# Kernel optimization log

Measured on AMD Instinct MI355X. Metric: run time of the kernel, lower is better.

Reference implementation:

```python
import jax, jax.numpy as jnp
from jax import lax
import numpy as np

RNN = 512; FC = 512; COND = 128; FEAT = 80; NCLS = 256; HALF = RNN // 2
PAD = 2; SCALES = (5, 5, 11); MEL_T = 86  # -> 22550 output samples


def setup_inputs() -> dict:
    key = jax.random.key(0)
    ks = jax.random.split(key, 12)
    s = 0.05
    p = {"mels": jax.random.normal(ks[0], (1, FEAT, MEL_T), jnp.float32)}
    ch = FEAT
    for i, sc in enumerate(SCALES):
        k = 2 * sc + 1
        p[f"up_w{i}"] = jax.random.normal(ks[1 + i], (COND, ch, k), jnp.float32) * s
        p[f"up_b{i}"] = jnp.zeros((COND,), jnp.float32)
        ch = COND
    p["Wx"] = jax.random.normal(ks[4], (3 * RNN, 3 + COND), jnp.float32) * s
    p["bx"] = jnp.zeros((3 * RNN,), jnp.float32)
    p["Wh"] = jax.random.normal(ks[5], (3 * RNN, RNN), jnp.float32) * s
    p["bh"] = jnp.zeros((3 * RNN,), jnp.float32)
    p["O1w"] = jax.random.normal(ks[6], (FC, HALF), jnp.float32) * s
    p["O1b"] = jnp.zeros((FC,), jnp.float32)
    p["O2w"] = jax.random.normal(ks[7], (NCLS, FC), jnp.float32) * s
    p["O2b"] = jnp.zeros((NCLS,), jnp.float32)
    p["O3w"] = jax.random.normal(ks[8], (FC, HALF), jnp.float32) * s
    p["O3b"] = jnp.zeros((FC,), jnp.float32)
    p["O4w"] = jax.random.normal(ks[9], (NCLS, FC), jnp.float32) * s
    p["O4b"] = jnp.zeros((NCLS,), jnp.float32)
    return p


def _upsample(mels, ws, bs):
    # mels[:, :, excess_pad:-excess_pad] with excess_pad = PAD - 1 = 1
    x = mels[:, :, PAD - 1:-(PAD - 1)]
    for w, b, sc in zip(ws, bs, SCALES):
        k = 2 * sc + 1
        # ConvTranspose1d(stride=sc, kernel=k, padding=(3*sc-1)//2) as an
        # input-dilated conv: edge pad = k-1-torch_pad = (sc+1)//2
        e = k - 1 - (3 * sc - 1) // 2
        x = lax.conv_general_dilated(x, w, window_strides=(1,),
                                     padding=[(e, e)], lhs_dilation=(sc,),
                                     dimension_numbers=('NCH', 'OIH', 'NCH'))
        x = jax.nn.relu(x + b[None, :, None])
    return x[0, :, 1:-1].T  # [T, COND]


def _gru(inp, h, Wx, bx, Wh, bh):
    xg = Wx @ inp + bx
    hg = Wh @ h + bh
    xr, xz, xn = jnp.split(xg, 3)
    hr, hz, hn = jnp.split(hg, 3)
    r = jax.nn.sigmoid(xr + hr)
    z = jax.nn.sigmoid(xz + hz)
    n = jnp.tanh(xn + r * hn)
    return (1.0 - z) * n + z * h


def reference(mels, up_w0, up_b0, up_w1, up_b1, up_w2, up_b2,
              Wx, bx, Wh, bh, O1w, O1b, O2w, O2b, O3w, O3b, O4w, O4b):
    cond = _upsample(mels, (up_w0, up_w1, up_w2), (up_b0, up_b1, up_b2))
    zero = jnp.float32(0.0)

    def step(carry, m_t):
        h, c_val, f_val = carry
        # coarse pass: x = [c_{t-1}, f_{t-1}, 0]
        inp1 = jnp.concatenate([jnp.stack([c_val, f_val, zero]), m_t])
        h1 = _gru(inp1, h, Wx, bx, Wh, bh)
        oc = O2w @ jax.nn.relu(O1w @ h1[:HALF] + O1b) + O2b
        c_cat = jnp.argmax(oc).astype(jnp.float32)  # deterministic=True path
        c_new = c_cat / 127.5 - 1.0
        # fine pass: x = [c_{t-1}, f_{t-1}, c_t]
        inp2 = jnp.concatenate([jnp.stack([c_val, f_val, c_new]), m_t])
        h2 = _gru(inp2, h, Wx, bx, Wh, bh)
        of = O4w @ jax.nn.relu(O3w @ h2[HALF:] + O3b) + O4b
        f_cat = jnp.argmax(of).astype(jnp.float32)
        f_new = f_cat / 127.5 - 1.0
        sample = (c_cat * 256.0 + f_cat) / 32767.5 - 1.0
        return (h2, c_new, f_new), (sample, jnp.concatenate([oc, of]))

    init = (jnp.zeros((RNN,), jnp.float32), zero, zero)
    _, (samples, logits) = lax.scan(step, init, cond)
    return samples, logits  # [T], [T, 512]
```

## Files before the change

kernel.cpp:

```cpp
#include <hip/hip_runtime.h>
#include <math.h>

#define T_STEPS 22550
#define NWG 32
#define NTHR 256

typedef unsigned long long ull;

#define SL_PRE  0
#define SL_O1   2048
#define SL_O3   2560
#define SL_AM1  3072
#define SL_AM2  3104
#define SL_END  3168

#define OF_SLOT  64
#define OF_AFTER (OF_SLOT + SL_END*2)
#define OF_BUFA  OF_AFTER
#define OF_BUFB  (OF_BUFA + 128*412)
#define OF_COND  (OF_BUFB + 128*2052)

__global__ void k_init(float* ws){
  int i = blockIdx.x*blockDim.x + threadIdx.x;
  ull* sl = (ull*)(ws + OF_SLOT);
  if (i < SL_END) __hip_atomic_store(&sl[i], 0ULL, __ATOMIC_RELAXED, __HIP_MEMORY_SCOPE_AGENT);
}

__global__ void k_upconv(const float* __restrict__ x, int instride, int inoff,
                         const float* __restrict__ w, const float* __restrict__ b,
                         float* __restrict__ y, int Cin, int Lin, int K, int sc, int e,
                         int Lout, int mode)
{
  int j = blockIdx.x*blockDim.x + threadIdx.x;
  int c = blockIdx.y;
  if (j >= Lout) return;
  float acc = b[c];
  int kstart = ((e - j) % sc + sc) % sc;
  for (int i = 0; i < Cin; ++i){
    const float* wci = w + (c*Cin + i)*K;
    const float* xi  = x + i*instride + inoff;
    for (int k = kstart; k < K; k += sc){
      int qd = j - e + k;
      if (qd >= 0){
        int qq = qd / sc;
        if (qq < Lin) acc += wci[k]*xi[qq];
      }
    }
  }
  acc = fmaxf(acc, 0.f);
  if (mode == 0) y[c*Lout + j] = acc;
  else { int t = j - 1; if (t >= 0 && t < T_STEPS) y[t*128 + c] = acc; }
}

__device__ __forceinline__ float sigm(float x){ return 1.f/(1.f + expf(-x)); }

__device__ __forceinline__ void pub64(ull* p, ull pk){
  (void)__hip_atomic_exchange(p, pk, __ATOMIC_RELAXED, __HIP_MEMORY_SCOPE_AGENT);
}
__device__ __forceinline__ ull ld64(ull* p){
  return __hip_atomic_load(p, __ATOMIC_RELAXED, __HIP_MEMORY_SCOPE_AGENT);
}
__device__ __forceinline__ float spin_data(ull* p, unsigned tag){
  ull pk = ld64(p);
  while ((unsigned)pk != tag) pk = ld64(p);
  return __uint_as_float((unsigned)(pk >> 32));
}
__device__ __forceinline__ ull spin_am(ull* p, unsigned tag){
  ull pk = ld64(p);
  while ((unsigned)(pk & 0xFFFFFFu) != tag) pk = ld64(p);
  return pk;
}
__device__ __forceinline__ ull pack_data(float v, unsigned tag){
  return ((ull)__float_as_uint(v) << 32) | (ull)tag;
}

__launch_bounds__(NTHR)
__global__ void k_wavernn(const float* __restrict__ Wx, const float* __restrict__ bx,
                          const float* __restrict__ Wh, const float* __restrict__ bh,
                          const float* __restrict__ O1w, const float* __restrict__ O1b,
                          const float* __restrict__ O2w, const float* __restrict__ O2b,
                          const float* __restrict__ O3w, const float* __restrict__ O3b,
                          const float* __restrict__ O4w, const float* __restrict__ O4b,
                          float* ws, float* __restrict__ out)
{
  __shared__ __align__(16) float h_s[512];
  __shared__ __align__(16) float m_s[128];
  __shared__ __align__(16) float h1_s[256];
  __shared__ __align__(16) float o_s[512];
  __shared__ __align__(16) float pr_s[512], pz_s[512], pna_s[512], hn_s[512];
  __shared__ __align__(16) float w1r_s[512], w1z_s[512], w1n_s[512];
  __shared__ __align__(16) float w2r_s[512], w2z_s[512], w2n_s[512];
  __shared__ float hg_s[48], xgb_s[48];
  __shared__ float red_s[8], sc_s[8];
  __shared__ float wc0_s[48], bx_s[48], bh_s[48];

  const int tid = threadIdx.x, g = blockIdx.x;
  ull* sl = (ull*)(ws + OF_SLOT);
  const float* cond = ws + OF_COND;
  float* out_samp = out;
  float* out_log  = out + T_STEPS;

  if (tid < 48){
    int row = (tid>>4)*512 + g + 32*(tid&15);
    wc0_s[tid] = Wx[(size_t)row*131 + 0];
    bx_s[tid]  = bx[row];
    bh_s[tid]  = bh[row];
  }
  for (int e = tid; e < 512; e += NTHR){
    w1r_s[e] = Wx[(size_t)e*131 + 1];
    w1z_s[e] = Wx[(size_t)(512+e)*131 + 1];
    w1n_s[e] = Wx[(size_t)(1024+e)*131 + 1];
    w2r_s[e] = Wx[(size_t)e*131 + 2];
    w2z_s[e] = Wx[(size_t)(512+e)*131 + 2];
    w2n_s[e] = Wx[(size_t)(1024+e)*131 + 2];
  }
  const int m16 = tid>>4, c16 = tid&15;
  const int rowO1 = g + 32*m16;
  float wO1r[16], wO3r[16];
  #pragma unroll
  for (int k=0;k<16;++k){
    wO1r[k] = O1w[(size_t)rowO1*256 + c16*16 + k];
    wO3r[k] = O3w[(size_t)rowO1*256 + c16*16 + k];
  }
  const float bO1r = O1b[rowO1], bO3r = O3b[rowO1];
  const int m8 = tid>>5, l32 = tid&31;
  const int row2 = g + 32*m8;
  float wO2r[16], wO4r[16];
  #pragma unroll
  for (int k=0;k<16;++k){
    wO2r[k] = O2w[(size_t)row2*512 + l32 + 32*k];
    wO4r[k] = O4w[(size_t)row2*512 + l32 + 32*k];
  }
  const float bO2 = O2b[row2], bO4 = O4b[row2];

  h_s[tid] = 0.f; h_s[tid+256] = 0.f;
  if (tid < 128) m_s[tid] = cond[tid];
  if (tid == 0){ sc_s[0] = 0.f; sc_s[2] = 0.f; sc_s[3] = 0.f; }
  __syncthreads();

  #define COMPUTE_WX() do { \
    if (tid < 192){ \
      const int li_ = tid>>2, q_ = tid&3; \
      const int row_ = (li_>>4)*512 + g + 32*(li_&15); \
      const float* WxR = Wx + (size_t)row_*131 + 3; \
      float aX = 0.f; \
      _Pragma("unroll") \
      for (int kk=0; kk<32; ++kk){ \
        int f_ = q_*32 + ((kk + 8*q_) & 31); \
        aX += WxR[f_]*m_s[f_]; \
      } \
      aX += __shfl_xor(aX,1); aX += __shfl_xor(aX,2); \
      if (q_ == 0) xgb_s[li_] = aX + bx_s[li_]; \
    } } while(0)

  #define COMPUTE_WH() do { \
    if (tid < 192){ \
      const int li_ = tid>>2, q_ = tid&3; \
      const int row_ = (li_>>4)*512 + g + 32*(li_&15); \
      const float4* W4 = (const float4*)(Wh + (size_t)row_*512); \
      const float4* H4 = (const float4*)h_s; \
      float aH = 0.f; \
      _Pragma("unroll") \
      for (int kk=0; kk<32; ++kk){ \
        int f_ = q_*32 + ((kk + 2*q_) & 31); \
        float4 w = W4[f_], v = H4[f_]; \
        aH += w.x*v.x + w.y*v.y + w.z*v.z + w.w*v.w; \
      } \
      aH += __shfl_xor(aH,1); aH += __shfl_xor(aH,2); \
      if (q_ == 0) hg_s[li_] = aH + bh_s[li_]; \
    } } while(0)

  #define PUB_PREGATES(TAGP) do { \
    if (tid < 64){ \
      const int i_ = tid>>2, c_ = tid&3; \
      const int e_ = g + 32*i_; \
      const float c0_ = sc_s[3]; \
      float v_; \
      if (c_ == 0)      v_ = xgb_s[i_]    + c0_*wc0_s[i_]    + hg_s[i_]; \
      else if (c_ == 1) v_ = xgb_s[16+i_] + c0_*wc0_s[16+i_] + hg_s[16+i_]; \
      else if (c_ == 2) v_ = xgb_s[32+i_] + c0_*wc0_s[32+i_]; \
      else              v_ = hg_s[32+i_]; \
      pub64(&sl[SL_PRE + e_*4 + c_], pack_data(v_, (TAGP))); \
    } } while(0)

  COMPUTE_WX();
  if (tid < 48) hg_s[tid] = bh_s[tid];
  __syncthreads();
  PUB_PREGATES(1u);

  for (int t = 0; t < T_STEPS; ++t){
    const unsigned tag = (unsigned)(t + 1);

    {
      ull pk[8];
      #pragma unroll
      for (int c=0;c<4;++c){
        pk[c]   = ld64(&sl[SL_PRE + tid*4 + c]);
        pk[4+c] = ld64(&sl[SL_PRE + (tid+256)*4 + c]);
      }
      bool all;
      do {
        all = true;
        #pragma unroll
        for (int i=0;i<8;++i){
          if ((unsigned)pk[i] != tag){
            int slot = (i<4) ? (tid*4 + i) : ((tid+256)*4 + (i-4));
            pk[i] = ld64(&sl[SL_PRE + slot]);
            if ((unsigned)pk[i] != tag) all = false;
          }
        }
      } while (!all);
      pr_s[tid]      = __uint_as_float((unsigned)(pk[0] >> 32));
      pz_s[tid]      = __uint_as_float((unsigned)(pk[1] >> 32));
      pna_s[tid]     = __uint_as_float((unsigned)(pk[2] >> 32));
      hn_s[tid]      = __uint_as_float((unsigned)(pk[3] >> 32));
      pr_s[tid+256]  = __uint_as_float((unsigned)(pk[4] >> 32));
      pz_s[tid+256]  = __uint_as_float((unsigned)(pk[5] >> 32));
      pna_s[tid+256] = __uint_as_float((unsigned)(pk[6] >> 32));
      hn_s[tid+256]  = __uint_as_float((unsigned)(pk[7] >> 32));
    }
    if (t > 0 && tid < 32){
      ull pk = spin_am(&sl[SL_AM2 + ((t-1) & 1)*32 + tid], tag - 1);
      float bv = __uint_as_float((unsigned)(pk >> 32));
      int   bi = (int)((pk >> 24) & 0xFFu);
      #pragma unroll
      for (int off=16; off>=1; off>>=1){
        float ov = __shfl_xor(bv,off); int oi = __shfl_xor(bi,off);
        if (ov > bv || (ov == bv && oi < bi)){ bv = ov; bi = oi; }
      }
      if (tid == 0){
        sc_s[0] = (float)bi/127.5f - 1.f;
        if (g == 0) out_samp[t-1] = (sc_s[2]*256.f + (float)bi)/32767.5f - 1.f;
      }
    }
    if (tid < 128 && t + 1 < T_STEPS) m_s[tid] = cond[(size_t)(t+1)*128 + tid];
    __syncthreads();

    {
      const float f = sc_s[0];
      float r = sigm(pr_s[tid]  + f*w1r_s[tid]);
      float z = sigm(pz_s[tid]  + f*w1z_s[tid]);
      float n = tanhf(pna_s[tid] + f*w1n_s[tid] + r*hn_s[tid]);
      h1_s[tid] = (1.f - z)*n + z*h_s[tid];
    }
    __syncthreads();

    {
      float acc = 0.f;
      #pragma unroll
      for (int k=0;k<16;++k) acc += wO1r[k]*h1_s[c16*16 + k];
      acc += __shfl_xor(acc,1); acc += __shfl_xor(acc,2);
      acc += __shfl_xor(acc,4); acc += __shfl_xor(acc,8);
      if (c16 == 0) pub64(&sl[SL_O1 + g*16 + m16], pack_data(fmaxf(acc + bO1r, 0.f), tag));
    }
    COMPUTE_WX();
    o_s[tid]       = spin_data(&sl[SL_O1 + (tid & 31)*16 + (tid >> 5)], tag);
    o_s[tid + 256] = spin_data(&sl[SL_O1 + (tid & 31)*16 + (tid >> 5) + 8], tag);
    __syncthreads();

    {
      float acc = 0.f;
      #pragma unroll
      for (int k=0;k<16;++k) acc += wO2r[k]*o_s[l32 + 32*k];
      acc += __shfl_xor(acc,1); acc += __shfl_xor(acc,2); acc += __shfl_xor(acc,4);
      acc += __shfl_xor(acc,8); acc += __shfl_xor(acc,16);
      if (l32 == 0){ float v = acc + bO2; out_log[(size_t)t*512 + row2] = v; red_s[m8] = v; }
    }
    __syncthreads();
    if (tid == 0){
      float bv = red_s[0]; int bi = g;
      #pragma unroll
      for (int m=1;m<8;++m){ float v = red_s[m]; if (v > bv){ bv = v; bi = g + 32*m; } }
      pub64(&sl[SL_AM1 + g],
            ((ull)__float_as_uint(bv) << 32) | ((ull)(unsigned)bi << 24) | tag);
    }
    if (tid < 32){
      ull pk = spin_am(&sl[SL_AM1 + tid], tag);
      float bv = __uint_as_float((unsigned)(pk >> 32));
      int   bi = (int)((pk >> 24) & 0xFFu);
      #pragma unroll
      for (int off=16; off>=1; off>>=1){
        float ov = __shfl_xor(bv,off); int oi = __shfl_xor(bi,off);
        if (ov > bv || (ov == bv && oi < bi)){ bv = ov; bi = oi; }
      }
      if (tid == 0){ sc_s[2] = (float)bi; sc_s[3] = (float)bi/127.5f - 1.f; }
    }
    __syncthreads();

    {
      const float f = sc_s[0], cn = sc_s[3];
      #pragma unroll
      for (int hh=0; hh<2; ++hh){
        int e = tid + 256*hh;
        float r = sigm(pr_s[e]  + f*w1r_s[e] + cn*w2r_s[e]);
        float z = sigm(pz_s[e]  + f*w1z_s[e] + cn*w2z_s[e]);
        float n = tanhf(pna_s[e] + f*w1n_s[e] + cn*w2n_s[e] + r*hn_s[e]);
        h_s[e] = (1.f - z)*n + z*h_s[e];
      }
    }
    __syncthreads();

    {
      float acc = 0.f;
      #pragma unroll
      for (int k=0;k<16;++k) acc += wO3r[k]*h_s[256 + c16*16 + k];
      acc += __shfl_xor(acc,1); acc += __shfl_xor(acc,2);
      acc += __shfl_xor(acc,4); acc += __shfl_xor(acc,8);
      if (c16 == 0) pub64(&sl[SL_O3 + g*16 + m16], pack_data(fmaxf(acc + bO3r, 0.f), tag));
    }
    COMPUTE_WH();
    __syncthreads();
    if (t + 1 < T_STEPS) PUB_PREGATES((unsigned)(t + 2));
    o_s[tid]       = spin_data(&sl[SL_O3 + (tid & 31)*16 + (tid >> 5)], tag);
    o_s[tid + 256] = spin_data(&sl[SL_O3 + (tid & 31)*16 + (tid >> 5) + 8], tag);
    __syncthreads();

    {
      float acc = 0.f;
      #pragma unroll
      for (int k=0;k<16;++k) acc += wO4r[k]*o_s[l32 + 32*k];
      acc += __shfl_xor(acc,1); acc += __shfl_xor(acc,2); acc += __shfl_xor(acc,4);
      acc += __shfl_xor(acc,8); acc += __shfl_xor(acc,16);
      if (l32 == 0){ float v = acc + bO4; out_log[(size_t)t*512 + 256 + row2] = v; red_s[m8] = v; }
    }
    __syncthreads();
    if (tid == 0){
      float bv = red_s[0]; int bi = g;
      #pragma unroll
      for (int m=1;m<8;++m){ float v = red_s[m]; if (v > bv){ bv = v; bi = g + 32*m; } }
      pub64(&sl[SL_AM2 + (t & 1)*32 + g],
            ((ull)__float_as_uint(bv) << 32) | ((ull)(unsigned)bi << 24) | tag);
    }
  }

  if (g == 0 && tid < 32){
    ull pk = spin_am(&sl[SL_AM2 + ((T_STEPS-1) & 1)*32 + tid], (unsigned)T_STEPS);
    float bv = __uint_as_float((unsigned)(pk >> 32));
    int   bi = (int)((pk >> 24) & 0xFFu);
    #pragma unroll
    for (int off=16; off>=1; off>>=1){
      float ov = __shfl_xor(bv,off); int oi = __shfl_xor(bi,off);
      if (ov > bv || (ov == bv && oi < bi)){ bv = ov; bi = oi; }
    }
    if (tid == 0) out_samp[T_STEPS-1] = (sc_s[2]*256.f + (float)bi)/32767.5f - 1.f;
  }
}

extern "C" void kernel_launch(void* const* d_in, const int* in_sizes, int n_in,
                              void* d_out, int out_size, void* d_ws, size_t ws_size,
                              hipStream_t stream)
{
  const float* mels  = (const float*)d_in[0];
  const float* up_w0 = (const float*)d_in[1]; const float* up_b0 = (const float*)d_in[2];
  const float* up_w1 = (const float*)d_in[3]; const float* up_b1 = (const float*)d_in[4];
  const float* up_w2 = (const float*)d_in[5]; const float* up_b2 = (const float*)d_in[6];
  const float* Wx  = (const float*)d_in[7];  const float* bx  = (const float*)d_in[8];
  const float* Wh  = (const float*)d_in[9];  const float* bh  = (const float*)d_in[10];
  const float* O1w = (const float*)d_in[11]; const float* O1b = (const float*)d_in[12];
  const float* O2w = (const float*)d_in[13]; const float* O2b = (const float*)d_in[14];
  const float* O3w = (const float*)d_in[15]; const float* O3b = (const float*)d_in[16];
  const float* O4w = (const float*)d_in[17]; const float* O4b = (const float*)d_in[18];
  float* ws  = (float*)d_ws;
  float* out = (float*)d_out;

  k_init<<<(SL_END + 255)/256, 256, 0, stream>>>(ws);

  k_upconv<<<dim3((412  +127)/128, 128), 128, 0, stream>>>(mels,        86,   1, up_w0, up_b0,
            ws+OF_BUFA,  80,   84, 11,  5, 3,   412, 0);
  k_upconv<<<dim3((2052 +127)/128, 128), 128, 0, stream>>>(ws+OF_BUFA, 412,   0, up_w1, up_b1,
            ws+OF_BUFB, 128,  412, 11,  5, 3,  2052, 0);
  k_upconv<<<dim3((22552+127)/128, 128), 128, 0, stream>>>(ws+OF_BUFB, 2052,  0, up_w2, up_b2,
            ws+OF_COND, 128, 2052, 23, 11, 6, 22552, 1);

  k_wavernn<<<NWG, NTHR, 0, stream>>>(Wx, bx, Wh, bh, O1w, O1b, O2w, O2b,
                                      O3w, O3b, O4w, O4b, ws, out);
}
```

Before: 295.9 ms.

## Replace two-phase O2/O4 exchange with partial-logit all-gather and local argmax

Each workgroup now multiplies its own 16 O1/O3 hidden units by the matching O2/O4 weight columns and publishes 256 partial logits. Every workgroup then gathers all 32 partials per logit and computes the full logits and argmax locally. This replaces the former chain of publishing hidden activations, spinning, computing logit slices, publishing per-group argmax and spinning again, cutting one cross-workgroup synchronisation round per pass. In exchange, each thread polls 32 slots per pass, which adds memory traffic and register pressure, and every group redundantly reduces all 256 logits.

```diff
diff --git a/kernel.cpp b/kernel.cpp
--- a/kernel.cpp
+++ b/kernel.cpp
@@ -8,11 +8,9 @@
 typedef unsigned long long ull;
 
 #define SL_PRE  0
-#define SL_O1   2048
-#define SL_O3   2560
-#define SL_AM1  3072
-#define SL_AM2  3104
-#define SL_END  3168
+#define SL_PLC  2048
+#define SL_PLF  10240
+#define SL_END  18432
 
 #define OF_SLOT  64
 #define OF_AFTER (OF_SLOT + SL_END*2)
@@ -60,16 +58,6 @@
 __device__ __forceinline__ ull ld64(ull* p){
   return __hip_atomic_load(p, __ATOMIC_RELAXED, __HIP_MEMORY_SCOPE_AGENT);
 }
-__device__ __forceinline__ float spin_data(ull* p, unsigned tag){
-  ull pk = ld64(p);
-  while ((unsigned)pk != tag) pk = ld64(p);
-  return __uint_as_float((unsigned)(pk >> 32));
-}
-__device__ __forceinline__ ull spin_am(ull* p, unsigned tag){
-  ull pk = ld64(p);
-  while ((unsigned)(pk & 0xFFFFFFu) != tag) pk = ld64(p);
-  return pk;
-}
 __device__ __forceinline__ ull pack_data(float v, unsigned tag){
   return ((ull)__float_as_uint(v) << 32) | (ull)tag;
 }
@@ -86,12 +74,13 @@
   __shared__ __align__(16) float h_s[512];
   __shared__ __align__(16) float m_s[128];
   __shared__ __align__(16) float h1_s[256];
-  __shared__ __align__(16) float o_s[512];
+  __shared__ __align__(16) float logit_s[256];
   __shared__ __align__(16) float pr_s[512], pz_s[512], pna_s[512], hn_s[512];
   __shared__ __align__(16) float w1r_s[512], w1z_s[512], w1n_s[512];
   __shared__ __align__(16) float w2r_s[512], w2z_s[512], w2n_s[512];
+  __shared__ float o1own_s[16], o3own_s[16];
   __shared__ float hg_s[48], xgb_s[48];
-  __shared__ float red_s[8], sc_s[8];
+  __shared__ float sc_s[8];
   __shared__ float wc0_s[48], bx_s[48], bh_s[48];
 
   const int tid = threadIdx.x, g = blockIdx.x;
@@ -123,15 +112,13 @@
     wO3r[k] = O3w[(size_t)rowO1*256 + c16*16 + k];
   }
   const float bO1r = O1b[rowO1], bO3r = O3b[rowO1];
-  const int m8 = tid>>5, l32 = tid&31;
-  const int row2 = g + 32*m8;
-  float wO2r[16], wO4r[16];
+  float wPC[16], wPF[16];
   #pragma unroll
-  for (int k=0;k<16;++k){
-    wO2r[k] = O2w[(size_t)row2*512 + l32 + 32*k];
-    wO4r[k] = O4w[(size_t)row2*512 + l32 + 32*k];
-  }
-  const float bO2 = O2b[row2], bO4 = O4b[row2];
+  for (int m=0;m<16;++m){
+    wPC[m] = O2w[(size_t)tid*512 + g + 32*m];
+    wPF[m] = O4w[(size_t)tid*512 + g + 32*m];
+  }
+  const float cbO2 = O2b[tid], cbO4 = O4b[tid];
 
   h_s[tid] = 0.f; h_s[tid+256] = 0.f;
   if (tid < 128) m_s[tid] = cond[tid];
@@ -183,6 +170,25 @@
       pub64(&sl[SL_PRE + e_*4 + c_], pack_data(v_, (TAGP))); \
     } } while(0)
 
+  #define FAT_GATHER(BASE, BIAS) do { \
+    ull pk_[32]; \
+    _Pragma("unroll") \
+    for (int g2=0; g2<32; ++g2) pk_[g2] = ld64(&sl[(BASE) + g2*256 + tid]); \
+    for (;;){ \
+      bool all_ = true; \
+      _Pragma("unroll") \
+      for (int g2=0; g2<32; ++g2) if ((unsigned)pk_[g2] != tag) all_ = false; \
+      if (all_) break; \
+      _Pragma("unroll") \
+      for (int g2=0; g2<32; ++g2) \
+        if ((unsigned)pk_[g2] != tag) pk_[g2] = ld64(&sl[(BASE) + g2*256 + tid]); \
+    } \
+    float s_ = (BIAS); \
+    _Pragma("unroll") \
+    for (int g2=0; g2<32; ++g2) s_ += __uint_as_float((unsigned)(pk_[g2] >> 32)); \
+    logit_s[tid] = s_; \
+  } while(0)
+
   COMPUTE_WX();
   if (tid < 48) hg_s[tid] = bh_s[tid];
   __syncthreads();
@@ -198,18 +204,18 @@
         pk[c]   = ld64(&sl[SL_PRE + tid*4 + c]);
         pk[4+c] = ld64(&sl[SL_PRE + (tid+256)*4 + c]);
       }
-      bool all;
-      do {
-        all = true;
+      for (;;){
+        bool all = true;
         #pragma unroll
-        for (int i=0;i<8;++i){
+        for (int i=0;i<8;++i) if ((unsigned)pk[i] != tag) all = false;
+        if (all) break;
+        #pragma unroll
+        for (int i=0;i<8;++i)
           if ((unsigned)pk[i] != tag){
             int slot = (i<4) ? (tid*4 + i) : ((tid+256)*4 + (i-4));
             pk[i] = ld64(&sl[SL_PRE + slot]);
-            if ((unsigned)pk[i] != tag) all = false;
           }
-        }
-      } while (!all);
+      }
       pr_s[tid]      = __uint_as_float((unsigned)(pk[0] >> 32));
       pz_s[tid]      = __uint_as_float((unsigned)(pk[1] >> 32));
       pna_s[tid]     = __uint_as_float((unsigned)(pk[2] >> 32));
@@ -219,20 +225,6 @@
       pna_s[tid+256] = __uint_as_float((unsigned)(pk[6] >> 32));
       hn_s[tid+256]  = __uint_as_float((unsigned)(pk[7] >> 32));
     }
-    if (t > 0 && tid < 32){
-      ull pk = spin_am(&sl[SL_AM2 + ((t-1) & 1)*32 + tid], tag - 1);
-      float bv = __uint_as_float((unsigned)(pk >> 32));
-      int   bi = (int)((pk >> 24) & 0xFFu);
-      #pragma unroll
-      for (int off=16; off>=1; off>>=1){
-        float ov = __shfl_xor(bv,off); int oi = __shfl_xor(bi,off);
-        if (ov > bv || (ov == bv && oi < bi)){ bv = ov; bi = oi; }
-      }
-      if (tid == 0){
-        sc_s[0] = (float)bi/127.5f - 1.f;
-        if (g == 0) out_samp[t-1] = (sc_s[2]*256.f + (float)bi)/32767.5f - 1.f;
-      }
-    }
     if (tid < 128 && t + 1 < T_STEPS) m_s[tid] = cond[(size_t)(t+1)*128 + tid];
     __syncthreads();
 
@@ -251,35 +243,27 @@
       for (int k=0;k<16;++k) acc += wO1r[k]*h1_s[c16*16 + k];
       acc += __shfl_xor(acc,1); acc += __shfl_xor(acc,2);
       acc += __shfl_xor(acc,4); acc += __shfl_xor(acc,8);
-      if (c16 == 0) pub64(&sl[SL_O1 + g*16 + m16], pack_data(fmaxf(acc + bO1r, 0.f), tag));
-    }
+      if (c16 == 0) o1own_s[m16] = fmaxf(acc + bO1r, 0.f);
+    }
+    __syncthreads();
+    {
+      float s = 0.f;
+      #pragma unroll
+      for (int m=0;m<16;++m) s += wPC[m]*o1own_s[m];
+      pub64(&sl[SL_PLC + g*256 + tid], pack_data(s, tag));
+    }
+
     COMPUTE_WX();
-    o_s[tid]       = spin_data(&sl[SL_O1 + (tid & 31)*16 + (tid >> 5)], tag);
-    o_s[tid + 256] = spin_data(&sl[SL_O1 + (tid & 31)*16 + (tid >> 5) + 8], tag);
-    __syncthreads();
-
-    {
-      float acc = 0.f;
-      #pragma unroll
-      for (int k=0;k<16;++k) acc += wO2r[k]*o_s[l32 + 32*k];
-      acc += __shfl_xor(acc,1); acc += __shfl_xor(acc,2); acc += __shfl_xor(acc,4);
-      acc += __shfl_xor(acc,8); acc += __shfl_xor(acc,16);
-      if (l32 == 0){ float v = acc + bO2; out_log[(size_t)t*512 + row2] = v; red_s[m8] = v; }
-    }
-    __syncthreads();
-    if (tid == 0){
-      float bv = red_s[0]; int bi = g;
-      #pragma unroll
-      for (int m=1;m<8;++m){ float v = red_s[m]; if (v > bv){ bv = v; bi = g + 32*m; } }
-      pub64(&sl[SL_AM1 + g],
-            ((ull)__float_as_uint(bv) << 32) | ((ull)(unsigned)bi << 24) | tag);
-    }
-    if (tid < 32){
-      ull pk = spin_am(&sl[SL_AM1 + tid], tag);
-      float bv = __uint_as_float((unsigned)(pk >> 32));
-      int   bi = (int)((pk >> 24) & 0xFFu);
-      #pragma unroll
-      for (int off=16; off>=1; off>>=1){
+
+    FAT_GATHER(SL_PLC, cbO2);
+    __syncthreads();
+    if (tid < 8) out_log[(size_t)t*512 + g*8 + tid] = logit_s[g*8 + tid];
+    if (tid < 64){
+      float bv = logit_s[tid]; int bi = tid;
+      #pragma unroll
+      for (int j=1;j<4;++j){ float v = logit_s[tid + 64*j]; if (v > bv){ bv = v; bi = tid + 64*j; } }
+      #pragma unroll
+      for (int off=32; off>=1; off>>=1){
         float ov = __shfl_xor(bv,off); int oi = __shfl_xor(bi,off);
         if (ov > bv || (ov == bv && oi < bi)){ bv = ov; bi = oi; }
       }
@@ -306,43 +290,37 @@
       for (int k=0;k<16;++k) acc += wO3r[k]*h_s[256 + c16*16 + k];
       acc += __shfl_xor(acc,1); acc += __shfl_xor(acc,2);
       acc += __shfl_xor(acc,4); acc += __shfl_xor(acc,8);
-      if (c16 == 0) pub64(&sl[SL_O3 + g*16 + m16], pack_data(fmaxf(acc + bO3r, 0.f), tag));
-    }
+      if (c16 == 0) o3own_s[m16] = fmaxf(acc + bO3r, 0.f);
+    }
+    __syncthreads();
+    {
+      float s = 0.f;
+      #pragma unroll
+      for (int m=0;m<16;++m) s += wPF[m]*o3own_s[m];
+      pub64(&sl[SL_PLF + g*256 + tid], pack_data(s, tag));
+    }
+
     COMPUTE_WH();
     __syncthreads();
     if (t + 1 < T_STEPS) PUB_PREGATES((unsigned)(t + 2));
-    o_s[tid]       = spin_data(&sl[SL_O3 + (tid & 31)*16 + (tid >> 5)], tag);
-    o_s[tid + 256] = spin_data(&sl[SL_O3 + (tid & 31)*16 + (tid >> 5) + 8], tag);
-    __syncthreads();
-
-    {
-      float acc = 0.f;
-      #pragma unroll
-      for (int k=0;k<16;++k) acc += wO4r[k]*o_s[l32 + 32*k];
-      acc += __shfl_xor(acc,1); acc += __shfl_xor(acc,2); acc += __shfl_xor(acc,4);
-      acc += __shfl_xor(acc,8); acc += __shfl_xor(acc,16);
-      if (l32 == 0){ float v = acc + bO4; out_log[(size_t)t*512 + 256 + row2] = v; red_s[m8] = v; }
-    }
-    __syncthreads();
-    if (tid == 0){
-      float bv = red_s[0]; int bi = g;
-      #pragma unroll
-      for (int m=1;m<8;++m){ float v = red_s[m]; if (v > bv){ bv = v; bi = g + 32*m; } }
-      pub64(&sl[SL_AM2 + (t & 1)*32 + g],
-            ((ull)__float_as_uint(bv) << 32) | ((ull)(unsigned)bi << 24) | tag);
-    }
-  }
-
-  if (g == 0 && tid < 32){
-    ull pk = spin_am(&sl[SL_AM2 + ((T_STEPS-1) & 1)*32 + tid], (unsigned)T_STEPS);
-    float bv = __uint_as_float((unsigned)(pk >> 32));
-    int   bi = (int)((pk >> 24) & 0xFFu);
-    #pragma unroll
-    for (int off=16; off>=1; off>>=1){
-      float ov = __shfl_xor(bv,off); int oi = __shfl_xor(bi,off);
-      if (ov > bv || (ov == bv && oi < bi)){ bv = ov; bi = oi; }
-    }
-    if (tid == 0) out_samp[T_STEPS-1] = (sc_s[2]*256.f + (float)bi)/32767.5f - 1.f;
+
+    FAT_GATHER(SL_PLF, cbO4);
+    __syncthreads();
+    if (tid < 8) out_log[(size_t)t*512 + 256 + g*8 + tid] = logit_s[g*8 + tid];
+    if (tid < 64){
+      float bv = logit_s[tid]; int bi = tid;
+      #pragma unroll
+      for (int j=1;j<4;++j){ float v = logit_s[tid + 64*j]; if (v > bv){ bv = v; bi = tid + 64*j; } }
+      #pragma unroll
+      for (int off=32; off>=1; off>>=1){
+        float ov = __shfl_xor(bv,off); int oi = __shfl_xor(bi,off);
+        if (ov > bv || (ov == bv && oi < bi)){ bv = ov; bi = oi; }
+      }
+      if (tid == 0){
+        sc_s[0] = (float)bi/127.5f - 1.f;
+        if (g == 0) out_samp[t] = (sc_s[2]*256.f + (float)bi)/32767.5f - 1.f;
+      }
+    }
   }
 }
 
```

Measured after the change: 295.9 ms. About the same (+0.0%).

## Co-locate persistent team on one XCD and spin on L2 with sc0 loads

Applied to the files above, without the earlier changes.

The launch now uses 256 workgroups, reads each block's XCC id from a hardware register, and elects the 32 blocks that share one XCC as the working team; the other blocks exit. When the team shares an XCC, the flag exchanges use non-coherent sc0 global loads and stores, meant to be served by that XCC's shared L2 instead of device-coherent memory. Every publish is also mirrored to an agent-scope atomic slot, which readers poll occasionally as a fallback. A generation counter replaces zeroing the flag slots on each launch. This targets the cross-workgroup handoff latency of the serial recurrence, at the cost of a startup election and handshake and a dependence on sc0 behaviour and on how blocks are placed across XCCs.

```diff
diff --git a/kernel.cpp b/kernel.cpp
--- a/kernel.cpp
+++ b/kernel.cpp
@@ -4,26 +4,39 @@
 #define T_STEPS 22550
 #define NWG 32
 #define NTHR 256
+#define GRID 256
 
 typedef unsigned long long ull;
+typedef unsigned int uint4v __attribute__((ext_vector_type(4)));
 
 #define SL_PRE  0
 #define SL_O1   2048
 #define SL_O3   2560
 #define SL_AM1  3072
 #define SL_AM2  3104
-#define SL_END  3168
-
-#define OF_SLOT  64
-#define OF_AFTER (OF_SLOT + SL_END*2)
-#define OF_BUFA  OF_AFTER
+#define SL_VER  3168
+#define SL_TOT  3200
+
+#define OF_GEN   8
+#define OF_ELEC  16
+#define OF_ARR   64
+#define OF_VOTE  320
+#define OF_FAST  384
+#define OF_MIR   6784
+#define OF_BUFA  13184
 #define OF_BUFB  (OF_BUFA + 128*412)
 #define OF_COND  (OF_BUFB + 128*2052)
 
 __global__ void k_init(float* ws){
   int i = blockIdx.x*blockDim.x + threadIdx.x;
-  ull* sl = (ull*)(ws + OF_SLOT);
-  if (i < SL_END) __hip_atomic_store(&sl[i], 0ULL, __ATOMIC_RELAXED, __HIP_MEMORY_SCOPE_AGENT);
+  if (i == 0){
+    unsigned* gen = (unsigned*)(ws + OF_GEN);
+    unsigned g = (__hip_atomic_load(gen, __ATOMIC_RELAXED, __HIP_MEMORY_SCOPE_AGENT) + 1u) & 0xFFFFFFu;
+    if (g == 0) g = 1;
+    __hip_atomic_store(gen, g, __ATOMIC_RELAXED, __HIP_MEMORY_SCOPE_AGENT);
+  }
+  if (i >= 8 && i < 16)
+    __hip_atomic_store((int*)(ws + OF_ELEC) + (i - 8), 0, __ATOMIC_RELAXED, __HIP_MEMORY_SCOPE_AGENT);
 }
 
 __global__ void k_upconv(const float* __restrict__ x, int instride, int inoff,
@@ -54,24 +67,78 @@
 
 __device__ __forceinline__ float sigm(float x){ return 1.f/(1.f + expf(-x)); }
 
-__device__ __forceinline__ void pub64(ull* p, ull pk){
-  (void)__hip_atomic_exchange(p, pk, __ATOMIC_RELAXED, __HIP_MEMORY_SCOPE_AGENT);
-}
-__device__ __forceinline__ ull ld64(ull* p){
-  return __hip_atomic_load(p, __ATOMIC_RELAXED, __HIP_MEMORY_SCOPE_AGENT);
-}
-__device__ __forceinline__ float spin_data(ull* p, unsigned tag){
-  ull pk = ld64(p);
-  while ((unsigned)pk != tag) pk = ld64(p);
-  return __uint_as_float((unsigned)(pk >> 32));
-}
-__device__ __forceinline__ ull spin_am(ull* p, unsigned tag){
-  ull pk = ld64(p);
-  while ((unsigned)(pk & 0xFFFFFFu) != tag) pk = ld64(p);
-  return pk;
+__device__ __forceinline__ ull ld64_f(const ull* p){
+  ull r;
+  asm volatile("global_load_dwordx2 %0, %1, off sc0\n\ts_waitcnt vmcnt(0)"
+               : "=&v"(r) : "v"(p) : "memory");
+  return r;
+}
+__device__ __forceinline__ void ld2_f(const ull* p0, const ull* p1, ull& a, ull& b){
+  asm volatile("global_load_dwordx2 %0, %2, off sc0\n\t"
+               "global_load_dwordx2 %1, %3, off sc0\n\t"
+               "s_waitcnt vmcnt(0)"
+               : "=&v"(a), "=&v"(b) : "v"(p0), "v"(p1) : "memory");
+}
+__device__ __forceinline__ void ld4_f(const ull* p, ull pk[4]){
+  uint4v a, b;
+  asm volatile("global_load_dwordx4 %0, %2, off sc0\n\t"
+               "global_load_dwordx4 %1, %3, off sc0\n\t"
+               "s_waitcnt vmcnt(0)"
+               : "=&v"(a), "=&v"(b) : "v"(p), "v"(p + 2) : "memory");
+  pk[0] = ((ull)a.y << 32) | a.x;  pk[1] = ((ull)a.w << 32) | a.z;
+  pk[2] = ((ull)b.y << 32) | b.x;  pk[3] = ((ull)b.w << 32) | b.z;
+}
+__device__ __forceinline__ void st64_f(ull* p, ull v){
+  asm volatile("global_store_dwordx2 %0, %1, off sc0" :: "v"(p), "v"(v) : "memory");
+}
+__device__ __forceinline__ ull ld64_a(const ull* p){
+  return __hip_atomic_load((ull*)p, __ATOMIC_RELAXED, __HIP_MEMORY_SCOPE_AGENT);
+}
+__device__ __forceinline__ void pub_dual(ull* f, ull* m, ull pk){
+  st64_f(f, pk);
+  __hip_atomic_store(m, pk, __ATOMIC_RELAXED, __HIP_MEMORY_SCOPE_AGENT);
 }
 __device__ __forceinline__ ull pack_data(float v, unsigned tag){
   return ((ull)__float_as_uint(v) << 32) | (ull)tag;
+}
+__device__ __forceinline__ ull spin_am_dual(ull* f, ull* m, unsigned tag, bool FM){
+  if (FM){
+    int it = 0;
+    for (;;){
+      ull pk = ld64_f(f);
+      if ((unsigned)(pk & 0xFFFFFFu) == tag) return pk;
+      if (((++it) & 15) == 0){
+        pk = ld64_a(m);
+        if ((unsigned)(pk & 0xFFFFFFu) == tag) return pk;
+      }
+    }
+  }
+  ull pk = ld64_a(m);
+  while ((unsigned)(pk & 0xFFFFFFu) != tag) pk = ld64_a(m);
+  return pk;
+}
+__device__ __forceinline__ void spin2_dual(ull* f0, ull* f1, ull* m0, ull* m1,
+                                           unsigned tag, bool FM, float& r0, float& r1){
+  ull v0 = 0, v1 = 0; unsigned done = 0;
+  if (FM){
+    int it = 0;
+    while (done != 3u){
+      ull a, b; ld2_f(f0, f1, a, b);
+      if (!(done & 1) && (unsigned)a == tag){ v0 = a; done |= 1; }
+      if (!(done & 2) && (unsigned)b == tag){ v1 = b; done |= 2; }
+      if (((++it) & 15) == 0){
+        if (!(done & 1)){ ull q = ld64_a(m0); if ((unsigned)q == tag){ v0 = q; done |= 1; } }
+        if (!(done & 2)){ ull q = ld64_a(m1); if ((unsigned)q == tag){ v1 = q; done |= 2; } }
+      }
+    }
+  } else {
+    while (done != 3u){
+      if (!(done & 1)){ ull q = ld64_a(m0); if ((unsigned)q == tag){ v0 = q; done |= 1; } }
+      if (!(done & 2)){ ull q = ld64_a(m1); if ((unsigned)q == tag){ v1 = q; done |= 2; } }
+    }
+  }
+  r0 = __uint_as_float((unsigned)(v0 >> 32));
+  r1 = __uint_as_float((unsigned)(v1 >> 32));
 }
 
 __launch_bounds__(NTHR)
@@ -93,12 +160,77 @@
   __shared__ float hg_s[48], xgb_s[48];
   __shared__ float red_s[8], sc_s[8];
   __shared__ float wc0_s[48], bx_s[48], bh_s[48];
-
-  const int tid = threadIdx.x, g = blockIdx.x;
-  ull* sl = (ull*)(ws + OF_SLOT);
+  __shared__ unsigned gen_sh;
+  __shared__ int team_sh, fastc_sh, saw_sh, fm_sh, myxcc_sh, myslot_sh;
+  __shared__ int cnt_sh[8];
+
+  const int tid = threadIdx.x;
+  int* elec = (int*)(ws + OF_ELEC);
+  unsigned* arr = (unsigned*)(ws + OF_ARR);
+  unsigned* vote = (unsigned*)(ws + OF_VOTE);
+  ull* fA = (ull*)(ws + OF_FAST);
+  ull* mA = (ull*)(ws + OF_MIR);
   const float* cond = ws + OF_COND;
   float* out_samp = out;
   float* out_log  = out + T_STEPS;
+
+  if (tid == 0){
+    gen_sh = __hip_atomic_load((unsigned*)(ws + OF_GEN), __ATOMIC_RELAXED, __HIP_MEMORY_SCOPE_AGENT);
+    unsigned xcc;
+    asm volatile("s_getreg_b32 %0, hwreg(20, 0, 4)" : "=s"(xcc));
+    myxcc_sh = (int)(xcc & 7u);
+    myslot_sh = __hip_atomic_fetch_add(&elec[xcc & 7u], 1, __ATOMIC_RELAXED, __HIP_MEMORY_SCOPE_AGENT);
+    __hip_atomic_store(&arr[blockIdx.x], gen_sh, __ATOMIC_RELAXED, __HIP_MEMORY_SCOPE_AGENT);
+  }
+  __syncthreads();
+  {
+    unsigned v;
+    do { v = __hip_atomic_load(&arr[tid], __ATOMIC_RELAXED, __HIP_MEMORY_SCOPE_AGENT); }
+    while (v != gen_sh);
+  }
+  __syncthreads();
+  if (tid < 8) cnt_sh[tid] = __hip_atomic_load(&elec[tid], __ATOMIC_RELAXED, __HIP_MEMORY_SCOPE_AGENT);
+  __syncthreads();
+  if (tid == 0){
+    int w = 0, c = -1;
+    for (int x = 0; x < 8; ++x) if (cnt_sh[x] > c){ c = cnt_sh[x]; w = x; }
+    if (c >= NWG){
+      fastc_sh = 1;
+      team_sh = (myxcc_sh == w && myslot_sh < NWG) ? myslot_sh : -1;
+    } else {
+      fastc_sh = 0;
+      team_sh = (blockIdx.x < NWG) ? (int)blockIdx.x : -1;
+    }
+  }
+  __syncthreads();
+  if (team_sh < 0) return;
+  const int g = team_sh;
+
+  if (fastc_sh){
+    if (tid == 0){ st64_f(&fA[SL_VER + g], (ull)gen_sh); saw_sh = 0; }
+    __syncthreads();
+    if (tid < 32){
+      bool ok = false;
+      for (int it = 0; it < 60000 && !ok; ++it)
+        ok = ((unsigned)ld64_f(&fA[SL_VER + tid]) == gen_sh);
+      ull mb = __ballot(ok);
+      if (tid == 0) saw_sh = (__popcll(mb) == 32);
+    }
+    __syncthreads();
+    if (tid == 0)
+      __hip_atomic_store(&vote[g], gen_sh | (saw_sh ? 0x1000000u : 0u),
+                         __ATOMIC_RELAXED, __HIP_MEMORY_SCOPE_AGENT);
+    if (tid < 32){
+      unsigned v;
+      do { v = __hip_atomic_load(&vote[tid], __ATOMIC_RELAXED, __HIP_MEMORY_SCOPE_AGENT); }
+      while ((v & 0xFFFFFFu) != gen_sh);
+      bool ok = (v >> 24) & 1u;
+      ull mb = __ballot(ok);
+      if (tid == 0) fm_sh = (__popcll(mb) == 32);
+    }
+  } else if (tid == 0) fm_sh = 0;
+  __syncthreads();
+  const bool FM = (fm_sh != 0);
 
   if (tid < 48){
     int row = (tid>>4)*512 + g + 32*(tid&15);
@@ -180,7 +312,8 @@
       else if (c_ == 1) v_ = xgb_s[16+i_] + c0_*wc0_s[16+i_] + hg_s[16+i_]; \
       else if (c_ == 2) v_ = xgb_s[32+i_] + c0_*wc0_s[32+i_]; \
       else              v_ = hg_s[32+i_]; \
-      pub64(&sl[SL_PRE + e_*4 + c_], pack_data(v_, (TAGP))); \
+      int sx_ = SL_PRE + e_*4 + c_; \
+      pub_dual(&fA[sx_], &mA[sx_], pack_data(v_, (TAGP))); \
     } } while(0)
 
   COMPUTE_WX();
@@ -192,35 +325,50 @@
     const unsigned tag = (unsigned)(t + 1);
 
     {
-      ull pk[8];
-      #pragma unroll
-      for (int c=0;c<4;++c){
-        pk[c]   = ld64(&sl[SL_PRE + tid*4 + c]);
-        pk[4+c] = ld64(&sl[SL_PRE + (tid+256)*4 + c]);
-      }
-      bool all;
-      do {
-        all = true;
-        #pragma unroll
-        for (int i=0;i<8;++i){
-          if ((unsigned)pk[i] != tag){
-            int slot = (i<4) ? (tid*4 + i) : ((tid+256)*4 + (i-4));
-            pk[i] = ld64(&sl[SL_PRE + slot]);
-            if ((unsigned)pk[i] != tag) all = false;
+      ull vs[8]; unsigned done = 0;
+      if (FM){
+        int it = 0;
+        while (done != 0xFFu){
+          ull pk[4];
+          ld4_f(&fA[SL_PRE + tid*4], pk);
+          #pragma unroll
+          for (int i=0;i<4;++i)
+            if (!((done>>i)&1) && (unsigned)pk[i]==tag){ vs[i]=pk[i]; done|=1u<<i; }
+          ld4_f(&fA[SL_PRE + (tid+256)*4], pk);
+          #pragma unroll
+          for (int i=0;i<4;++i)
+            if (!((done>>(4+i))&1) && (unsigned)pk[i]==tag){ vs[4+i]=pk[i]; done|=1u<<(4+i); }
+          if (((++it) & 15) == 0 && done != 0xFFu){
+            #pragma unroll
+            for (int i=0;i<8;++i) if (!((done>>i)&1)){
+              int sx = (i<4) ? (tid*4+i) : ((tid+256)*4 + (i-4));
+              ull q = ld64_a(&mA[SL_PRE + sx]);
+              if ((unsigned)q == tag){ vs[i]=q; done|=1u<<i; }
+            }
           }
         }
-      } while (!all);
-      pr_s[tid]      = __uint_as_float((unsigned)(pk[0] >> 32));
-      pz_s[tid]      = __uint_as_float((unsigned)(pk[1] >> 32));
-      pna_s[tid]     = __uint_as_float((unsigned)(pk[2] >> 32));
-      hn_s[tid]      = __uint_as_float((unsigned)(pk[3] >> 32));
-      pr_s[tid+256]  = __uint_as_float((unsigned)(pk[4] >> 32));
-      pz_s[tid+256]  = __uint_as_float((unsigned)(pk[5] >> 32));
-      pna_s[tid+256] = __uint_as_float((unsigned)(pk[6] >> 32));
-      hn_s[tid+256]  = __uint_as_float((unsigned)(pk[7] >> 32));
+      } else {
+        while (done != 0xFFu){
+          #pragma unroll
+          for (int i=0;i<8;++i) if (!((done>>i)&1)){
+            int sx = (i<4) ? (tid*4+i) : ((tid+256)*4 + (i-4));
+            ull q = ld64_a(&mA[SL_PRE + sx]);
+            if ((unsigned)q == tag){ vs[i]=q; done|=1u<<i; }
+          }
+        }
+      }
+      pr_s[tid]      = __uint_as_float((unsigned)(vs[0] >> 32));
+      pz_s[tid]      = __uint_as_float((unsigned)(vs[1] >> 32));
+      pna_s[tid]     = __uint_as_float((unsigned)(vs[2] >> 32));
+      hn_s[tid]      = __uint_as_float((unsigned)(vs[3] >> 32));
+      pr_s[tid+256]  = __uint_as_float((unsigned)(vs[4] >> 32));
+      pz_s[tid+256]  = __uint_as_float((unsigned)(vs[5] >> 32));
+      pna_s[tid+256] = __uint_as_float((unsigned)(vs[6] >> 32));
+      hn_s[tid+256]  = __uint_as_float((unsigned)(vs[7] >> 32));
     }
     if (t > 0 && tid < 32){
-      ull pk = spin_am(&sl[SL_AM2 + ((t-1) & 1)*32 + tid], tag - 1);
+      int sx = SL_AM2 + ((t-1) & 1)*32 + tid;
+      ull pk = spin_am_dual(&fA[sx], &mA[sx], tag - 1, FM);
       float bv = __uint_as_float((unsigned)(pk >> 32));
       int   bi = (int)((pk >> 24) & 0xFFu);
       #pragma unroll
@@ -251,11 +399,16 @@
       for (int k=0;k<16;++k) acc += wO1r[k]*h1_s[c16*16 + k];
       acc += __shfl_xor(acc,1); acc += __shfl_xor(acc,2);
       acc += __shfl_xor(acc,4); acc += __shfl_xor(acc,8);
-      if (c16 == 0) pub64(&sl[SL_O1 + g*16 + m16], pack_data(fmaxf(acc + bO1r, 0.f), tag));
+      if (c16 == 0){
+        int sx = SL_O1 + g*16 + m16;
+        pub_dual(&fA[sx], &mA[sx], pack_data(fmaxf(acc + bO1r, 0.f), tag));
+      }
     }
     COMPUTE_WX();
-    o_s[tid]       = spin_data(&sl[SL_O1 + (tid & 31)*16 + (tid >> 5)], tag);
-    o_s[tid + 256] = spin_data(&sl[SL_O1 + (tid & 31)*16 + (tid >> 5) + 8], tag);
+    {
+      int s0 = SL_O1 + (tid & 31)*16 + (tid >> 5);
+      spin2_dual(&fA[s0], &fA[s0+8], &mA[s0], &mA[s0+8], tag, FM, o_s[tid], o_s[tid+256]);
+    }
     __syncthreads();
 
     {
@@ -271,11 +424,11 @@
       float bv = red_s[0]; int bi = g;
       #pragma unroll
       for (int m=1;m<8;++m){ float v = red_s[m]; if (v > bv){ bv = v; bi = g + 32*m; } }
-      pub64(&sl[SL_AM1 + g],
-            ((ull)__float_as_uint(bv) << 32) | ((ull)(unsigned)bi << 24) | tag);
+      ull pk = ((ull)__float_as_uint(bv) << 32) | ((ull)(unsigned)bi << 24) | tag;
+      pub_dual(&fA[SL_AM1 + g], &mA[SL_AM1 + g], pk);
     }
     if (tid < 32){
-      ull pk = spin_am(&sl[SL_AM1 + tid], tag);
+      ull pk = spin_am_dual(&fA[SL_AM1 + tid], &mA[SL_AM1 + tid], tag, FM);
       float bv = __uint_as_float((unsigned)(pk >> 32));
       int   bi = (int)((pk >> 24) & 0xFFu);
       #pragma unroll
@@ -306,13 +459,18 @@
       for (int k=0;k<16;++k) acc += wO3r[k]*h_s[256 + c16*16 + k];
       acc += __shfl_xor(acc,1); acc += __shfl_xor(acc,2);
       acc += __shfl_xor(acc,4); acc += __shfl_xor(acc,8);
-      if (c16 == 0) pub64(&sl[SL_O3 + g*16 + m16], pack_data(fmaxf(acc + bO3r, 0.f), tag));
+      if (c16 == 0){
+        int sx = SL_O3 + g*16 + m16;
+        pub_dual(&fA[sx], &mA[sx], pack_data(fmaxf(acc + bO3r, 0.f), tag));
+      }
     }
     COMPUTE_WH();
     __syncthreads();
     if (t + 1 < T_STEPS) PUB_PREGATES((unsigned)(t + 2));
-    o_s[tid]       = spin_data(&sl[SL_O3 + (tid & 31)*16 + (tid >> 5)], tag);
-    o_s[tid + 256] = spin_data(&sl[SL_O3 + (tid & 31)*16 + (tid >> 5) + 8], tag);
+    {
+      int s0 = SL_O3 + (tid & 31)*16 + (tid >> 5);
+      spin2_dual(&fA[s0], &fA[s0+8], &mA[s0], &mA[s0+8], tag, FM, o_s[tid], o_s[tid+256]);
+    }
     __syncthreads();
 
     {
@@ -328,13 +486,15 @@
       float bv = red_s[0]; int bi = g;
       #pragma unroll
       for (int m=1;m<8;++m){ float v = red_s[m]; if (v > bv){ bv = v; bi = g + 32*m; } }
-      pub64(&sl[SL_AM2 + (t & 1)*32 + g],
-            ((ull)__float_as_uint(bv) << 32) | ((ull)(unsigned)bi << 24) | tag);
+      ull pk = ((ull)__float_as_uint(bv) << 32) | ((ull)(unsigned)bi << 24) | tag;
+      int sx = SL_AM2 + (t & 1)*32 + g;
+      pub_dual(&fA[sx], &mA[sx], pk);
     }
   }
 
   if (g == 0 && tid < 32){
-    ull pk = spin_am(&sl[SL_AM2 + ((T_STEPS-1) & 1)*32 + tid], (unsigned)T_STEPS);
+    int sx = SL_AM2 + ((T_STEPS-1) & 1)*32 + tid;
+    ull pk = spin_am_dual(&fA[sx], &mA[sx], (unsigned)T_STEPS, FM);
     float bv = __uint_as_float((unsigned)(pk >> 32));
     int   bi = (int)((pk >> 24) & 0xFFu);
     #pragma unroll
@@ -363,7 +523,7 @@
   float* ws  = (float*)d_ws;
   float* out = (float*)d_out;
 
-  k_init<<<(SL_END + 255)/256, 256, 0, stream>>>(ws);
+  k_init<<<1, 64, 0, stream>>>(ws);
 
   k_upconv<<<dim3((412  +127)/128, 128), 128, 0, stream>>>(mels,        86,   1, up_w0, up_b0,
             ws+OF_BUFA,  80,   84, 11,  5, 3,   412, 0);
@@ -372,6 +532,6 @@
   k_upconv<<<dim3((22552+127)/128, 128), 128, 0, stream>>>(ws+OF_BUFB, 2052,  0, up_w2, up_b2,
             ws+OF_COND, 128, 2052, 23, 11, 6, 22552, 1);
 
-  k_wavernn<<<NWG, NTHR, 0, stream>>>(Wx, bx, Wh, bh, O1w, O1b, O2w, O2b,
-                                      O3w, O3b, O4w, O4b, ws, out);
-}
+  k_wavernn<<<GRID, NTHR, 0, stream>>>(Wx, bx, Wh, bh, O1w, O1b, O2w, O2b,
+                                       O3w, O3b, O4w, O4b, ws, out);
+}
```

New measurement: 516.1 ms. 1.74x slower.
